# Kernel tuning notes

Hardware: AMD Instinct MI355X
Metric: run time of the kernel (lower is better)

## Reference

```python
import jax, jax.numpy as jnp
import numpy as np

EPS = 1e-6
SIGMA_C = 2.0
PAD = 0
VOCAB = 100
D_EMB = 384


def setup_inputs() -> dict:
    key = jax.random.key(0)
    k1, k2, k3 = jax.random.split(key, 3)
    B, L = 32, 1025  # L odd so durs[:,1::2] and durs[:,2::2] align
    text = jax.random.randint(k1, (B, L), 0, VOCAB)
    durs = jax.random.randint(k2, (B, L), 0, 4)
    emb_table = jax.random.normal(k3, (VOCAB, D_EMB), dtype=jnp.float32)
    return {"text": text, "durs": durs, "emb_table": emb_table, "total_time": 2048}


def reference(text, durs, emb_table, total_time):
    # --- merge blank/token pairs (as in GaussianEmbedding.forward) ---
    text_m = jnp.concatenate([text[:, :1], text[:, 1::2]], axis=1)              # [B,N]
    durs_m = jnp.concatenate([durs[:, :1], durs[:, 1::2] + durs[:, 2::2]], axis=1)  # [B,N]
    embed = emb_table[text_m]                                                    # [B,N,E]

    # --- Gaussian length regulation ---
    d = durs_m.astype(jnp.float32)
    cum = jnp.cumsum(d, axis=-1)                 # [B,N] end times
    c = cum - 0.5 * d                            # [B,N] token centers
    sig = d / SIGMA_C + EPS                      # [B,N]
    t = jnp.arange(total_time, dtype=jnp.float32) + 0.5  # [T] frame midpoints

    # Normal pdf weights [B,T,N]
    z = (t[None, :, None] - c[:, None, :]) / sig[:, None, :]
    w = jnp.exp(-0.5 * z * z) / (sig[:, None, :] * jnp.sqrt(2.0 * jnp.pi))
    # zero weight for pad tokens, normalize over tokens
    w = jnp.where((text_m == PAD)[:, None, :], 0.0, w)
    w = w / (w.sum(-1, keepdims=True) + EPS)
    # zero frames beyond each sample's total duration
    valid = t[None, :] < cum[:, -1:]             # [B,T]
    w = jnp.where(valid[..., None], w, 0.0)

    return jnp.einsum('btn,bne->bte', w, embed)  # [B,T,E]
```

## Files before the change

kernel.cpp:

```cpp
#include <hip/hip_runtime.h>
#include <hip/hip_bf16.h>

#define BATCH 32
#define LSEQ 1025
#define TT 2048
#define NTOK 513
#define EMB 384
#define FT 32
#define WMAX 120
#define INV_SQRT_2PI 0.3989422804014327f

__device__ inline float* scan513(float* src, float* dst) {
  for (int off = 1; off < NTOK; off <<= 1) {
    for (int i = threadIdx.x; i < NTOK; i += 256) {
      float v = src[i];
      if (i >= off) v += src[i - off];
      dst[i] = v;
    }
    __syncthreads();
    float* t = src; src = dst; dst = t;
  }
  return src;
}

__global__ __launch_bounds__(256) void prep_kernel(
    const int* __restrict__ text, const int* __restrict__ durs,
    float2* __restrict__ kept, int* __restrict__ counts,
    float* __restrict__ totals) {
  const int b = blockIdx.x;
  const int tid = threadIdx.x;
  __shared__ float s_a[NTOK], s_b[NTOK];
  __shared__ float s_c[NTOK];
  __shared__ float s_d[NTOK];
  __shared__ int s_tok[NTOK];

  const int* tb = text + b * LSEQ;
  const int* db = durs + b * LSEQ;
  for (int n = tid; n < NTOK; n += 256) {
    int dm, tk;
    if (n == 0) { dm = db[0]; tk = tb[0]; }
    else { dm = db[2 * n - 1] + db[2 * n]; tk = tb[2 * n - 1]; }
    s_d[n] = (float)dm;
    s_a[n] = (float)dm;
    s_tok[n] = tk;
  }
  __syncthreads();
  float* cum = scan513(s_a, s_b);
  for (int n = tid; n < NTOK; n += 256) {
    s_c[n] = cum[n] - 0.5f * s_d[n];
  }
  if (tid == 0) totals[b] = cum[NTOK - 1];
  __syncthreads();
  float* flagbuf = (cum == s_a) ? s_a : s_b;
  float* other = (cum == s_a) ? s_b : s_a;
  for (int n = tid; n < NTOK; n += 256) {
    flagbuf[n] = (s_d[n] >= 1.0f && s_tok[n] != 0) ? 1.0f : 0.0f;
  }
  __syncthreads();
  float* incl = scan513(flagbuf, other);
  for (int n = tid; n < NTOK; n += 256) {
    float d = s_d[n];
    int tk = s_tok[n];
    if (d >= 1.0f && tk != 0) {
      int pos = (int)incl[n] - 1;
      int packed = ((int)d << 17) | (tk * EMB);
      kept[b * NTOK + pos] = make_float2(s_c[n], __int_as_float(packed));
    }
  }
  if (tid == 0) counts[b] = (int)incl[NTOK - 1];
}

__global__ __launch_bounds__(192) void frames_kernel(
    const float2* __restrict__ kept, const int* __restrict__ counts,
    const float* __restrict__ totals, const float* __restrict__ emb,
    float* __restrict__ out) {
  const int t0 = blockIdx.x * FT;
  const int b = blockIdx.y;
  const int tid = threadIdx.x;

  __shared__ float4 s_tk[WMAX];
  __shared__ float s_reach[WMAX];
  __shared__ float s_w[WMAX * FT];
  __shared__ float s_factor[FT];

  const int M = counts[b];
  const float total = totals[b];
  const float2* kb = kept + b * NTOK;

  const float loB = (float)t0 - 39.5f;
  const float hiB = (float)t0 + (float)(FT - 1) + 40.5f;
  int l = 0, r = M;
  while (l < r) { int m = (l + r) >> 1; if (kb[m].x < loB) l = m + 1; else r = m; }
  const int lo = l;
  r = M;
  while (l < r) { int m = (l + r) >> 1; if (kb[m].x <= hiB) l = m + 1; else r = m; }
  int win = l - lo;
  if (win > WMAX) win = WMAX;

  for (int i = tid; i < win; i += 192) {
    float2 kv = kb[lo + i];
    int packed = __float_as_int(kv.y);
    int d = packed >> 17;
    int off = packed & 0x1FFFF;
    float df = (float)d;
    float inv_sig = 1.0f / (0.5f * df + 1e-6f);
    s_tk[i] = make_float4(kv.x, inv_sig, INV_SQRT_2PI * inv_sig,
                          __int_as_float(off));
    s_reach[i] = 6.7f * df + 1e-4f;
  }
  __syncthreads();

  const float t0f = (float)t0 + 0.5f;
  const int pairs = win * FT;
  for (int idx = tid; idx < pairs; idx += 192) {
    const int n = idx >> 5, f = idx & (FT - 1);
    const float4 tk = s_tk[n];
    const float z = (t0f + (float)f - tk.x) * tk.y;
    s_w[idx] = tk.z * __expf(-0.5f * z * z);
  }
  __syncthreads();

  if (tid < FT) {
    float s = 0.f;
    for (int n = 0; n < win; ++n) s += s_w[n * FT + tid];
    const float tf = t0f + (float)tid;
    s_factor[tid] = (tf < total) ? 1.0f / (s + 1e-6f) : 0.0f;
  }
  __syncthreads();

  const int fh = tid / 96;
  const int cg = (tid % 96) * 4;
  const int fbase = fh * 16;
  float4 acc[16];
#pragma unroll
  for (int k = 0; k < 16; ++k) acc[k] = make_float4(0.f, 0.f, 0.f, 0.f);

  const float fLo = (float)(t0 + fbase) + 0.5f;
  const float fHi = fLo + 15.0f;
  for (int n = 0; n < win; ++n) {
    const float4 tk = s_tk[n];
    const float reach = s_reach[n];
    if (tk.x + reach < fLo || tk.x - reach > fHi) continue;
    const int off = __float_as_int(tk.w);
    const float4 v = *(const float4*)(emb + off + cg);
    const float4* wp = (const float4*)(s_w + n * FT + fbase);
#pragma unroll
    for (int q = 0; q < 4; ++q) {
      const float4 w4 = wp[q];
      float4& a0 = acc[4 * q + 0];
      a0.x += w4.x * v.x; a0.y += w4.x * v.y; a0.z += w4.x * v.z; a0.w += w4.x * v.w;
      float4& a1 = acc[4 * q + 1];
      a1.x += w4.y * v.x; a1.y += w4.y * v.y; a1.z += w4.y * v.z; a1.w += w4.y * v.w;
      float4& a2 = acc[4 * q + 2];
      a2.x += w4.z * v.x; a2.y += w4.z * v.y; a2.z += w4.z * v.z; a2.w += w4.z * v.w;
      float4& a3 = acc[4 * q + 3];
      a3.x += w4.w * v.x; a3.y += w4.w * v.y; a3.z += w4.w * v.z; a3.w += w4.w * v.w;
    }
  }

  const size_t obase = ((size_t)b * TT + t0 + fbase) * EMB + cg;
#pragma unroll
  for (int k = 0; k < 16; ++k) {
    const float fac = s_factor[fbase + k];
    float4 r;
    r.x = acc[k].x * fac; r.y = acc[k].y * fac;
    r.z = acc[k].z * fac; r.w = acc[k].w * fac;
    *(float4*)(out + obase + (size_t)k * EMB) = r;
  }
}

extern "C" void kernel_launch(void* const* d_in, const int* in_sizes, int n_in,
                              void* d_out, int out_size, void* d_ws,
                              size_t ws_size, hipStream_t stream) {
  const int* text = (const int*)d_in[0];
  const int* durs = (const int*)d_in[1];
  const float* emb = (const float*)d_in[2];
  float* out = (float*)d_out;

  float2* kept = (float2*)d_ws;
  int* counts = (int*)(kept + BATCH * NTOK);
  float* totals = (float*)(counts + BATCH);

  prep_kernel<<<BATCH, 256, 0, stream>>>(text, durs, kept, counts, totals);
  frames_kernel<<<dim3(TT / FT, BATCH), 192, 0, stream>>>(kept, counts, totals,
                                                          emb, out);
}
```

Before: 134.4 us.

## Use wave-shuffle scans, precompute tile windows, and retile frames kernel to 256 threads

The prep kernel's shared-memory Hillis-Steele scans become register plus wave-shuffle scans. It now also precomputes each frame tile's token window with a binary search over the kept centres, so the frames kernel no longer searches global memory. The frames kernel moves to 256 threads, each handling 4 frames by 12 channels. The window margins, WMAX and per-token reach are tightened from about 6.7 sigma to 4 sigma, which lowers work but could drop small tail contributions and change accuracy slightly.

```diff
diff --git a/kernel.cpp b/kernel.cpp
--- a/kernel.cpp
+++ b/kernel.cpp
@@ -7,74 +7,107 @@
 #define NTOK 513
 #define EMB 384
 #define FT 32
-#define WMAX 120
+#define NTILE (TT / FT)
+#define WMAX 88
 #define INV_SQRT_2PI 0.3989422804014327f
-
-__device__ inline float* scan513(float* src, float* dst) {
-  for (int off = 1; off < NTOK; off <<= 1) {
-    for (int i = threadIdx.x; i < NTOK; i += 256) {
-      float v = src[i];
-      if (i >= off) v += src[i - off];
-      dst[i] = v;
-    }
-    __syncthreads();
-    float* t = src; src = dst; dst = t;
-  }
-  return src;
-}
 
 __global__ __launch_bounds__(256) void prep_kernel(
     const int* __restrict__ text, const int* __restrict__ durs,
-    float2* __restrict__ kept, int* __restrict__ counts,
+    float2* __restrict__ kept, int2* __restrict__ tile_win,
     float* __restrict__ totals) {
   const int b = blockIdx.x;
   const int tid = threadIdx.x;
-  __shared__ float s_a[NTOK], s_b[NTOK];
-  __shared__ float s_c[NTOK];
-  __shared__ float s_d[NTOK];
-  __shared__ int s_tok[NTOK];
+  const int lane = tid & 63;
+  const int wv = tid >> 6;
+
+  __shared__ float s_cc[NTOK];
+  __shared__ float s_wd[4], s_wf[4];
 
   const int* tb = text + b * LSEQ;
   const int* db = durs + b * LSEQ;
-  for (int n = tid; n < NTOK; n += 256) {
-    int dm, tk;
-    if (n == 0) { dm = db[0]; tk = tb[0]; }
-    else { dm = db[2 * n - 1] + db[2 * n]; tk = tb[2 * n - 1]; }
-    s_d[n] = (float)dm;
-    s_a[n] = (float)dm;
-    s_tok[n] = tk;
-  }
-  __syncthreads();
-  float* cum = scan513(s_a, s_b);
-  for (int n = tid; n < NTOK; n += 256) {
-    s_c[n] = cum[n] - 0.5f * s_d[n];
-  }
-  if (tid == 0) totals[b] = cum[NTOK - 1];
-  __syncthreads();
-  float* flagbuf = (cum == s_a) ? s_a : s_b;
-  float* other = (cum == s_a) ? s_b : s_a;
-  for (int n = tid; n < NTOK; n += 256) {
-    flagbuf[n] = (s_d[n] >= 1.0f && s_tok[n] != 0) ? 1.0f : 0.0f;
-  }
-  __syncthreads();
-  float* incl = scan513(flagbuf, other);
-  for (int n = tid; n < NTOK; n += 256) {
-    float d = s_d[n];
-    int tk = s_tok[n];
-    if (d >= 1.0f && tk != 0) {
-      int pos = (int)incl[n] - 1;
-      int packed = ((int)d << 17) | (tk * EMB);
-      kept[b * NTOK + pos] = make_float2(s_c[n], __int_as_float(packed));
+
+  float d[3], fl[3];
+  int tk[3];
+  const int nbase = 3 * tid;
+#pragma unroll
+  for (int j = 0; j < 3; ++j) {
+    const int n = nbase + j;
+    int dm = 0, t = 0;
+    if (n < NTOK) {
+      if (n == 0) { dm = db[0]; t = tb[0]; }
+      else { dm = db[2 * n - 1] + db[2 * n]; t = tb[2 * n - 1]; }
     }
-  }
-  if (tid == 0) counts[b] = (int)incl[NTOK - 1];
-}
-
-__global__ __launch_bounds__(192) void frames_kernel(
-    const float2* __restrict__ kept, const int* __restrict__ counts,
+    d[j] = (float)dm;
+    tk[j] = t;
+    fl[j] = (dm >= 1 && t != 0) ? 1.0f : 0.0f;
+  }
+  const float ld1 = d[0] + d[1], ld2 = ld1 + d[2];
+  const float lf1 = fl[0] + fl[1], lf2 = lf1 + fl[2];
+
+  float sd = ld2, sf = lf2;
+#pragma unroll
+  for (int off = 1; off < 64; off <<= 1) {
+    const float od = __shfl_up(sd, off);
+    const float of = __shfl_up(sf, off);
+    if (lane >= off) { sd += od; sf += of; }
+  }
+  if (lane == 63) { s_wd[wv] = sd; s_wf[wv] = sf; }
+  __syncthreads();
+
+  float wod = 0.f, wof = 0.f;
+#pragma unroll
+  for (int k = 0; k < 4; ++k) {
+    if (k < wv) { wod += s_wd[k]; wof += s_wf[k]; }
+  }
+  const float exd = wod + sd - ld2;
+  const float exf = wof + sf - lf2;
+
+  const float cum0 = exd + d[0], cum1 = exd + ld1, cum2 = exd + ld2;
+  const float fin0 = exf + fl[0], fin1 = exf + lf1, fin2 = exf + lf2;
+  const float cums[3] = {cum0, cum1, cum2};
+  const float fins[3] = {fin0, fin1, fin2};
+
+#pragma unroll
+  for (int j = 0; j < 3; ++j) {
+    const int n = nbase + j;
+    if (n < NTOK && fl[j] > 0.f) {
+      const int pos = (int)fins[j] - 1;
+      const float c = cums[j] - 0.5f * d[j];
+      const int packed = ((int)d[j] << 17) | (tk[j] * EMB);
+      kept[b * NTOK + pos] = make_float2(c, __int_as_float(packed));
+      s_cc[pos] = c;
+    }
+  }
+  const float total = s_wd[0] + s_wd[1] + s_wd[2] + s_wd[3];
+  const int M = (int)(s_wf[0] + s_wf[1] + s_wf[2] + s_wf[3]);
+  if (tid == 0) totals[b] = total;
+  __syncthreads();
+
+  if (tid < NTILE) {
+    const int t0 = tid * FT;
+    const float loB = (float)t0 - 23.6f;
+    const float hiB = (float)t0 + 55.6f;
+    int l = 0, r = M;
+    while (l < r) { const int m = (l + r) >> 1; if (s_cc[m] < loB) l = m + 1; else r = m; }
+    const int lo = l;
+    r = M;
+    while (l < r) { const int m = (l + r) >> 1; if (s_cc[m] <= hiB) l = m + 1; else r = m; }
+    int wn = l - lo;
+    if (wn > WMAX) wn = WMAX;
+    tile_win[b * NTILE + tid] = make_int2(lo, wn);
+  }
+}
+
+__device__ inline void fma4(float4& a, const float w, const float4 v) {
+  a.x += w * v.x; a.y += w * v.y; a.z += w * v.z; a.w += w * v.w;
+}
+
+__global__ __launch_bounds__(256) void frames_kernel(
+    const float2* __restrict__ kept, const int2* __restrict__ tile_win,
     const float* __restrict__ totals, const float* __restrict__ emb,
     float* __restrict__ out) {
-  const int t0 = blockIdx.x * FT;
+  const int tile = blockIdx.x;
+  const int t0 = tile * FT;
   const int b = blockIdx.y;
   const int tid = threadIdx.x;
 
@@ -83,36 +116,27 @@
   __shared__ float s_w[WMAX * FT];
   __shared__ float s_factor[FT];
 
-  const int M = counts[b];
   const float total = totals[b];
+  const int2 wininfo = tile_win[b * NTILE + tile];
+  const int lo = wininfo.x;
+  const int win = wininfo.y;
   const float2* kb = kept + b * NTOK;
 
-  const float loB = (float)t0 - 39.5f;
-  const float hiB = (float)t0 + (float)(FT - 1) + 40.5f;
-  int l = 0, r = M;
-  while (l < r) { int m = (l + r) >> 1; if (kb[m].x < loB) l = m + 1; else r = m; }
-  const int lo = l;
-  r = M;
-  while (l < r) { int m = (l + r) >> 1; if (kb[m].x <= hiB) l = m + 1; else r = m; }
-  int win = l - lo;
-  if (win > WMAX) win = WMAX;
-
-  for (int i = tid; i < win; i += 192) {
-    float2 kv = kb[lo + i];
-    int packed = __float_as_int(kv.y);
-    int d = packed >> 17;
-    int off = packed & 0x1FFFF;
-    float df = (float)d;
-    float inv_sig = 1.0f / (0.5f * df + 1e-6f);
+  for (int i = tid; i < win; i += 256) {
+    const float2 kv = kb[lo + i];
+    const int packed = __float_as_int(kv.y);
+    const int dI = packed >> 17;
+    const float df = (float)dI;
+    const float inv_sig = 1.0f / (0.5f * df + 1e-6f);
     s_tk[i] = make_float4(kv.x, inv_sig, INV_SQRT_2PI * inv_sig,
-                          __int_as_float(off));
-    s_reach[i] = 6.7f * df + 1e-4f;
+                          __int_as_float(packed & 0x1FFFF));
+    s_reach[i] = 4.0f * df + 1e-4f;
   }
   __syncthreads();
 
   const float t0f = (float)t0 + 0.5f;
-  const int pairs = win * FT;
-  for (int idx = tid; idx < pairs; idx += 192) {
+  const int pairs = win << 5;
+  for (int idx = tid; idx < pairs; idx += 256) {
     const int n = idx >> 5, f = idx & (FT - 1);
     const float4 tk = s_tk[n];
     const float z = (t0f + (float)f - tk.x) * tk.y;
@@ -122,50 +146,57 @@
 
   if (tid < FT) {
     float s = 0.f;
-    for (int n = 0; n < win; ++n) s += s_w[n * FT + tid];
+    for (int n = 0; n < win; ++n) s += s_w[(n << 5) + tid];
     const float tf = t0f + (float)tid;
     s_factor[tid] = (tf < total) ? 1.0f / (s + 1e-6f) : 0.0f;
   }
   __syncthreads();
 
-  const int fh = tid / 96;
-  const int cg = (tid % 96) * 4;
-  const int fbase = fh * 16;
-  float4 acc[16];
-#pragma unroll
-  for (int k = 0; k < 16; ++k) acc[k] = make_float4(0.f, 0.f, 0.f, 0.f);
-
-  const float fLo = (float)(t0 + fbase) + 0.5f;
-  const float fHi = fLo + 15.0f;
+  const int g = tid >> 5;
+  const int c = (tid & 31) * 12;
+  float4 acc[4][3];
+#pragma unroll
+  for (int j = 0; j < 4; ++j) {
+#pragma unroll
+    for (int k = 0; k < 3; ++k) acc[j][k] = make_float4(0.f, 0.f, 0.f, 0.f);
+  }
+
+  const float fLo = t0f + (float)(4 * g);
+  const float fHi = fLo + 3.0f;
   for (int n = 0; n < win; ++n) {
     const float4 tk = s_tk[n];
-    const float reach = s_reach[n];
-    if (tk.x + reach < fLo || tk.x - reach > fHi) continue;
+    const float rc = s_reach[n];
+    if (tk.x + rc < fLo || tk.x - rc > fHi) continue;
     const int off = __float_as_int(tk.w);
-    const float4 v = *(const float4*)(emb + off + cg);
-    const float4* wp = (const float4*)(s_w + n * FT + fbase);
-#pragma unroll
-    for (int q = 0; q < 4; ++q) {
-      const float4 w4 = wp[q];
-      float4& a0 = acc[4 * q + 0];
-      a0.x += w4.x * v.x; a0.y += w4.x * v.y; a0.z += w4.x * v.z; a0.w += w4.x * v.w;
-      float4& a1 = acc[4 * q + 1];
-      a1.x += w4.y * v.x; a1.y += w4.y * v.y; a1.z += w4.y * v.z; a1.w += w4.y * v.w;
-      float4& a2 = acc[4 * q + 2];
-      a2.x += w4.z * v.x; a2.y += w4.z * v.y; a2.z += w4.z * v.z; a2.w += w4.z * v.w;
-      float4& a3 = acc[4 * q + 3];
-      a3.x += w4.w * v.x; a3.y += w4.w * v.y; a3.z += w4.w * v.z; a3.w += w4.w * v.w;
+    const float4 w4 = *(const float4*)(s_w + (n << 5) + 4 * g);
+    const float4 v0 = *(const float4*)(emb + off + c);
+    const float4 v1 = *(const float4*)(emb + off + c + 4);
+    const float4 v2 = *(const float4*)(emb + off + c + 8);
+    const float wv_[4] = {w4.x, w4.y, w4.z, w4.w};
+#pragma unroll
+    for (int j = 0; j < 4; ++j) {
+      const float w = wv_[j];
+      fma4(acc[j][0], w, v0);
+      fma4(acc[j][1], w, v1);
+      fma4(acc[j][2], w, v2);
     }
   }
 
-  const size_t obase = ((size_t)b * TT + t0 + fbase) * EMB + cg;
-#pragma unroll
-  for (int k = 0; k < 16; ++k) {
-    const float fac = s_factor[fbase + k];
-    float4 r;
-    r.x = acc[k].x * fac; r.y = acc[k].y * fac;
-    r.z = acc[k].z * fac; r.w = acc[k].w * fac;
-    *(float4*)(out + obase + (size_t)k * EMB) = r;
+  float* op = out + ((size_t)b * TT + t0 + 4 * g) * EMB + c;
+#pragma unroll
+  for (int j = 0; j < 4; ++j) {
+    const float fac = s_factor[4 * g + j];
+    float* row = op + (size_t)j * EMB;
+    float4 r0, r1, r2;
+    r0.x = acc[j][0].x * fac; r0.y = acc[j][0].y * fac;
+    r0.z = acc[j][0].z * fac; r0.w = acc[j][0].w * fac;
+    r1.x = acc[j][1].x * fac; r1.y = acc[j][1].y * fac;
+    r1.z = acc[j][1].z * fac; r1.w = acc[j][1].w * fac;
+    r2.x = acc[j][2].x * fac; r2.y = acc[j][2].y * fac;
+    r2.z = acc[j][2].z * fac; r2.w = acc[j][2].w * fac;
+    *(float4*)(row) = r0;
+    *(float4*)(row + 4) = r1;
+    *(float4*)(row + 8) = r2;
   }
 }
 
@@ -178,10 +209,10 @@
   float* out = (float*)d_out;
 
   float2* kept = (float2*)d_ws;
-  int* counts = (int*)(kept + BATCH * NTOK);
-  float* totals = (float*)(counts + BATCH);
-
-  prep_kernel<<<BATCH, 256, 0, stream>>>(text, durs, kept, counts, totals);
-  frames_kernel<<<dim3(TT / FT, BATCH), 192, 0, stream>>>(kept, counts, totals,
-                                                          emb, out);
-}
+  int2* tile_win = (int2*)(kept + BATCH * NTOK);
+  float* totals = (float*)(tile_win + BATCH * NTILE);
+
+  prep_kernel<<<BATCH, 256, 0, stream>>>(text, durs, kept, tile_win, totals);
+  frames_kernel<<<dim3(NTILE, BATCH), 256, 0, stream>>>(kept, tile_win, totals,
+                                                        emb, out);
+}
```

After: 131.4 us. -2.2%, faster.
